# Optimization experiments

Hardware: AMD Instinct MI355X
Metric: run time of the kernel (lower is better)

## Reference

```python
import jax, jax.numpy as jnp
import numpy as np
from jax import lax

D_MODEL = 128
D_INNER = 256   # expand * d_model
D_STATE = 16
D_CONV = 4
DT_RANK = 8     # ceil(d_model / 16)
IN_CH = 64
SCALE = 0.02


def setup_inputs() -> dict:
    key = jax.random.key(0)
    ks = jax.random.split(key, 16)
    r = lambda k, s: jax.random.normal(k, s, dtype=jnp.float32)
    return {
        "x": r(ks[0], (4, IN_CH, 128, 128)),
        "conv_w": r(ks[1], (D_MODEL, IN_CH, 3, 3)) * SCALE,
        "conv_b": r(ks[2], (D_MODEL,)) * SCALE,
        "bn_g": jnp.ones((D_MODEL,), jnp.float32),
        "bn_b": jnp.zeros((D_MODEL,), jnp.float32),
        "bn_mean": r(ks[3], (D_MODEL,)) * SCALE,
        "bn_var": jax.random.uniform(ks[4], (D_MODEL,), jnp.float32) + 0.5,
        "in_w": r(ks[5], (2 * D_INNER, D_MODEL)) * SCALE,
        "conv1d_w": r(ks[6], (D_INNER, 1, D_CONV)) * SCALE,
        "conv1d_b": r(ks[7], (D_INNER,)) * SCALE,
        "xproj_w": r(ks[8], (DT_RANK + 2 * D_STATE, D_INNER)) * SCALE,
        "dtproj_w": r(ks[9], (D_INNER, DT_RANK)) * SCALE,
        "dtproj_b": r(ks[10], (D_INNER,)) * SCALE,
        "A_log": r(ks[11], (D_INNER, D_STATE)) * 0.5,
        "Dp": r(ks[12], (D_INNER,)) * SCALE,
        "out_w": r(ks[13], (D_MODEL, D_INNER)) * SCALE,
    }


def _mamba(u, in_w, conv1d_w, conv1d_b, xproj_w, dtproj_w, dtproj_b, A_log, Dp, out_w):
    # u: [B, L, d_model]
    xz = jnp.einsum("bld,ed->ble", u, in_w)          # [B, L, 2*d_inner]
    x_in, z = jnp.split(xz, 2, axis=-1)
    # depthwise causal conv1d over L
    xc = lax.conv_general_dilated(
        x_in.transpose(0, 2, 1), conv1d_w, (1,), [(D_CONV - 1, 0)],
        dimension_numbers=("NCL", "OIL", "NCL"), feature_group_count=D_INNER,
    ) + conv1d_b[None, :, None]
    x_in = jax.nn.silu(xc).transpose(0, 2, 1)         # [B, L, d_inner]

    x_dbl = jnp.einsum("bld,ed->ble", x_in, xproj_w)  # [B, L, dt_rank+2*d_state]
    dt, Bm, Cm = jnp.split(x_dbl, [DT_RANK, DT_RANK + D_STATE], axis=-1)
    delta = jax.nn.softplus(jnp.einsum("blr,dr->bld", dt, dtproj_w) + dtproj_b)

    A = -jnp.exp(A_log)                               # [d_inner, d_state]
    deltaA = jnp.exp(jnp.einsum("bld,dn->bldn", delta, A))        # [B,L,d,n]
    deltaBu = jnp.einsum("bld,bln,bld->bldn", delta, Bm, x_in)    # [B,L,d,n]

    def step(h, inp):
        dA, dBu, c = inp                              # [B,d,n],[B,d,n],[B,n]
        h = dA * h + dBu
        y = jnp.einsum("bdn,bn->bd", h, c)
        return h, y

    Bsz, L = u.shape[0], u.shape[1]
    h0 = jnp.zeros((Bsz, D_INNER, D_STATE), u.dtype)
    _, ys = lax.scan(step, h0, (deltaA.transpose(1, 0, 2, 3),
                                deltaBu.transpose(1, 0, 2, 3),
                                Cm.transpose(1, 0, 2)))
    y = ys.transpose(1, 0, 2) + x_in * Dp             # [B, L, d_inner]
    y = y * jax.nn.silu(z)
    return jnp.einsum("bld,ed->ble", y, out_w)        # [B, L, d_model]


def reference(x, conv_w, conv_b, bn_g, bn_b, bn_mean, bn_var, in_w, conv1d_w,
              conv1d_b, xproj_w, dtproj_w, dtproj_b, A_log, Dp, out_w):
    # downsample: conv3x3 stride2 + BN(eval) + exact GELU
    y = lax.conv_general_dilated(x, conv_w, (2, 2), [(1, 1), (1, 1)],
                                 dimension_numbers=("NCHW", "OIHW", "NCHW"))
    y = y + conv_b[None, :, None, None]
    inv = bn_g / jnp.sqrt(bn_var + 1e-5)
    y = (y - bn_mean[None, :, None, None]) * inv[None, :, None, None] + bn_b[None, :, None, None]
    y = jax.nn.gelu(y, approximate=False)             # [B, C, H, W]

    B, C, H, W = y.shape
    u = y.reshape(B, C, H * W).transpose(0, 2, 1)     # [B, L, C]
    out = _mamba(u, in_w, conv1d_w, conv1d_b, xproj_w, dtproj_w, dtproj_b,
                 A_log, Dp, out_w)
    out = out.transpose(0, 2, 1).reshape(B, C, H, W)
    return y + out
```

## Files before the change

kernel.cpp:

```cpp
#include <hip/hip_runtime.h>
#include <math.h>

#define NB 4
#define LTOK 4096
#define DM 128
#define DI 256
#define NCH 256
#define TCH 16
#define GSZ 16
#define NG  16

#define OFF_A2     0u
#define OFF_BIAS2  73728u
#define OFF_YDSR   84096u
#define OFF_XPRE   2181248u
#define OFF_Z      6375552u
#define OFF_DELTA  10569856u
#define OFF_YABF   12667008u
#define OFF_BC     14764160u
#define OFF_DSUM   15288448u
#define OFF_GS     15550592u
#define OFF_GD     15812736u
#define OFF_XT     15829120u
#define OFF_WBF    17926272u
#define OFF_WCMP   17963136u
#define OFF_YDSBF  18004096u
#define OFF_INWBF  19052672u
#define OFF_OUTWBF 19085440u

#define DEV __device__ __forceinline__
#define L2E 1.4426950408889634f

typedef short bh8 __attribute__((ext_vector_type(8)));
typedef float f4v __attribute__((ext_vector_type(4)));

DEV float fast_silu(float v) {
  return v * __builtin_amdgcn_rcpf(1.f + __expf(-v));
}

DEV unsigned short f2bf(float f) {
  unsigned int u = __float_as_uint(f);
  u = (u + 0x7FFFu + ((u >> 16) & 1u)) >> 16;
  return (unsigned short)u;
}

DEV float bf2f(unsigned short us) {
  return __uint_as_float((unsigned int)us << 16);
}

__global__ __launch_bounds__(256) void k0_prep(
    const float* __restrict__ conv_w, const float* __restrict__ conv_b,
    const float* __restrict__ bn_g, const float* __restrict__ bn_b,
    const float* __restrict__ bn_mean, const float* __restrict__ bn_var,
    const float* __restrict__ xproj_w, const float* __restrict__ A_log,
    const float* __restrict__ dtw, const float* __restrict__ in_w,
    const float* __restrict__ out_w, float* __restrict__ ws) {
  int i = blockIdx.x * 256 + threadIdx.x;
  if (i < 73728) {
    int ci = i & 63; int tap = (i >> 6) % 9; int co = i / 576;
    float inv = bn_g[co] * rsqrtf(bn_var[co] + 1e-5f);
    ((unsigned short*)(ws + OFF_WBF))[i] = f2bf(conv_w[co * 576 + ci * 9 + tap] * inv);
  } else if (i < 73856) {
    int co = i - 73728;
    float inv = bn_g[co] * rsqrtf(bn_var[co] + 1e-5f);
    ws[OFF_BIAS2 + co] = (conv_b[co] - bn_mean[co]) * inv + bn_b[co];
  } else if (i < 77952) {
    int j = i - 73856;
    ws[OFF_A2 + j] = -__expf(A_log[j]) * L2E;
  } else if (i < 159872) {
    int j = i - 77952;
    int n = j >> 8, k = j & 255;
    float v = 0.f;
    if (n < 256) {
#pragma unroll
      for (int r = 0; r < 8; ++r)
        v = fmaf(dtw[n * 8 + r], xproj_w[r * 256 + k], v);
    } else if (n < 288) {
      v = xproj_w[(8 + n - 256) * 256 + k];
    }
    ((unsigned short*)(ws + OFF_WCMP))[j] = f2bf(v);
  } else if (i < 225408) {
    int j = i - 159872;
    ((unsigned short*)(ws + OFF_INWBF))[j] = f2bf(in_w[j]);
  } else if (i < 258176) {
    int j = i - 225408;
    ((unsigned short*)(ws + OFF_OUTWBF))[j] = f2bf(out_w[j]);
  }
}

__global__ __launch_bounds__(256) void k0b_transpose(
    const float* __restrict__ x, unsigned short* __restrict__ xt) {
  __shared__ float t[64][65];
  const int tid = threadIdx.x;
  const int ixh = blockIdx.x & 1;
  const int iy = (blockIdx.x >> 1) & 127;
  const int b = blockIdx.x >> 8;
  {
    const int ixl = tid & 63, cw = tid >> 6;
#pragma unroll 4
    for (int i = 0; i < 16; ++i) {
      int ci = cw * 16 + i;
      t[ci][ixl] = x[(((size_t)(b * 64 + ci) * 128) + iy) * 128 + ixh * 64 + ixl];
    }
  }
  __syncthreads();
  {
    const int cil = tid & 63, iw = tid >> 6;
    unsigned short* dst = xt + (((size_t)(b * 128 + iy) * 128) + ixh * 64) * 64;
#pragma unroll 4
    for (int i = 0; i < 16; ++i) {
      int ix = iw * 16 + i;
      dst[ix * 64 + cil] = f2bf(t[cil][ix]);
    }
  }
}

__global__ __launch_bounds__(256) void k1_conv_mfma(
    const unsigned short* __restrict__ xt, const unsigned short* __restrict__ wbf,
    const float* __restrict__ bias2, unsigned short* __restrict__ ydsr,
    unsigned short* __restrict__ ydsbf) {
  __shared__ unsigned short ldt[64][66];
  const int tid = threadIdx.x;
  const int lane = tid & 63;
  const int w = tid >> 6;
  const int col = lane & 15, quad = lane >> 4;
  const int cohalf = blockIdx.x & 1;
  const int oy = (blockIdx.x >> 1) & 63;
  const int b = blockIdx.x >> 7;
  const int co0 = cohalf * 64 + (w & 1) * 32;
  const int tok0 = (w >> 1) * 32;
  const int iy0 = 2 * oy - 1;
  const bh8 bzero = {};
  f4v acc[2][2];
#pragma unroll
  for (int mt = 0; mt < 2; ++mt)
#pragma unroll
    for (int nt = 0; nt < 2; ++nt) acc[mt][nt] = (f4v){0.f, 0.f, 0.f, 0.f};

  const unsigned short* ap0 = wbf + (size_t)(co0 + col) * 576;
  const unsigned short* ap1 = wbf + (size_t)(co0 + 16 + col) * 576;

  for (int tap = 0; tap < 9; ++tap) {
    const int kh = tap / 3, kw = tap - kh * 3;
    const int iy = iy0 + kh;
    const int ix0 = 2 * (tok0 + col) - 1 + kw;
    const int ix1 = ix0 + 32;
    const unsigned short* xrow = xt + (long)(b * 128 + iy) * 8192;
    const bool ok0 = (iy >= 0) && (ix0 >= 0);
    const bool ok1 = (iy >= 0);
#pragma unroll
    for (int kc = 0; kc < 2; ++kc) {
      const int cib = kc * 32 + quad * 8;
      bh8 a0 = *(const bh8*)&ap0[tap * 64 + cib];
      bh8 a1 = *(const bh8*)&ap1[tap * 64 + cib];
      bh8 b0 = *(const bh8*)&xrow[(long)ix0 * 64 + cib];
      bh8 b1 = *(const bh8*)&xrow[(long)ix1 * 64 + cib];
      if (!ok0) b0 = bzero;
      if (!ok1) b1 = bzero;
      acc[0][0] = __builtin_amdgcn_mfma_f32_16x16x32_bf16(a0, b0, acc[0][0], 0, 0, 0);
      acc[1][0] = __builtin_amdgcn_mfma_f32_16x16x32_bf16(a1, b0, acc[1][0], 0, 0, 0);
      acc[0][1] = __builtin_amdgcn_mfma_f32_16x16x32_bf16(a0, b1, acc[0][1], 0, 0, 0);
      acc[1][1] = __builtin_amdgcn_mfma_f32_16x16x32_bf16(a1, b1, acc[1][1], 0, 0, 0);
    }
  }
#pragma unroll
  for (int mt = 0; mt < 2; ++mt)
#pragma unroll
    for (int nt = 0; nt < 2; ++nt) {
      const int tok = tok0 + nt * 16 + col;
#pragma unroll
      for (int r = 0; r < 4; ++r) {
        const int co = co0 + mt * 16 + quad * 4 + r;
        float v = acc[mt][nt][r] + bias2[co];
        float g = 0.5f * v * (1.f + erff(v * 0.70710678118f));
        unsigned short gb = f2bf(g);
        ydsr[(((size_t)(b * 128 + co) * 64) + oy) * 64 + tok] = gb;
        ldt[tok][(w & 1) * 32 + mt * 16 + quad * 4 + r] = gb;
      }
    }
  __syncthreads();
  {
    const int tok = tid >> 2, cg = (tid & 3) * 16;
    unsigned short* dst =
        ydsbf + ((size_t)(b * 4096 + oy * 64 + tok)) * 128 + cohalf * 64 + cg;
#pragma unroll
    for (int j = 0; j < 8; ++j)
      ((unsigned int*)dst)[j] = *(const unsigned int*)&ldt[tok][cg + 2 * j];
  }
}

__global__ __launch_bounds__(256) void k2_mfma(
    const unsigned short* __restrict__ ydsbf, const unsigned short* __restrict__ inwbf,
    unsigned short* __restrict__ xpre, unsigned short* __restrict__ z) {
  const int tid = threadIdx.x;
  const int lane = tid & 63;
  const int w = tid >> 6;
  const int col = lane & 15, quad = lane >> 4;
  const int tt = blockIdx.x & 255, b = blockIdx.x >> 8;
  const int t0 = tt * 16;
  bh8 afrag[4];
  {
    const unsigned short* arow = ydsbf + (size_t)(b * 4096 + t0 + col) * 128 + quad * 8;
#pragma unroll
    for (int kb = 0; kb < 4; ++kb) afrag[kb] = *(const bh8*)&arow[kb * 32];
  }
  f4v acc[8];
#pragma unroll
  for (int j = 0; j < 8; ++j) acc[j] = (f4v){0.f, 0.f, 0.f, 0.f};
  const int nt0 = w * 8;
  const unsigned short* wb = inwbf + (size_t)(nt0 * 16 + col) * 128 + quad * 8;
#pragma unroll
  for (int kb = 0; kb < 4; ++kb) {
#pragma unroll
    for (int j = 0; j < 8; ++j) {
      bh8 bfrag = *(const bh8*)&wb[(size_t)j * 2048 + kb * 32];
      acc[j] = __builtin_amdgcn_mfma_f32_16x16x32_bf16(afrag[kb], bfrag, acc[j], 0, 0, 0);
    }
  }
#pragma unroll
  for (int j = 0; j < 8; ++j) {
    const int e = (nt0 + j) * 16 + col;
#pragma unroll
    for (int r = 0; r < 4; ++r) {
      const int t = t0 + quad * 4 + r;
      if (e < 256) xpre[((size_t)(b * 4096 + t)) * 256 + e] = f2bf(acc[j][r]);
      else z[((size_t)(b * 4096 + t)) * 256 + e - 256] = f2bf(acc[j][r]);
    }
  }
}

__global__ __launch_bounds__(256) void k4_mfma(
    const unsigned short* __restrict__ wcomp, const float* __restrict__ dtb,
    const unsigned short* __restrict__ xpre, const float* __restrict__ cw1,
    const float* __restrict__ cb1, unsigned short* __restrict__ xinbf,
    unsigned short* __restrict__ delta, float* __restrict__ bc,
    float* __restrict__ dsum) {
  __shared__ unsigned short ld_xin[16][264];
  __shared__ unsigned short ld_delta[16][264];
  __shared__ float ld_bc[16][33];
  const int tid = threadIdx.x;
  const int lane = tid & 63;
  const int w = tid >> 6;
  const int col = lane & 15, quad = lane >> 4;
  const int tt = blockIdx.x & 255, b = blockIdx.x >> 8;
  const int t0 = tt * 16;

  {
    const int d = tid;
    float4 w4 = *(const float4*)&cw1[d * 4];
    float bias = cb1[d];
    float xw[19];
#pragma unroll
    for (int i = 0; i < 19; ++i) {
      int t = t0 - 3 + i;
      xw[i] = (t >= 0) ? bf2f(xpre[((size_t)(b * 4096 + t)) * 256 + d]) : 0.f;
    }
    unsigned short* dst = xinbf + ((size_t)(b * 4096 + t0)) * 256 + d;
#pragma unroll
    for (int i = 0; i < 16; ++i) {
      float o = bias + w4.x * xw[i] + w4.y * xw[i + 1] + w4.z * xw[i + 2] +
                w4.w * xw[i + 3];
      unsigned short us = f2bf(fast_silu(o));
      ld_xin[i][d] = us;
      dst[(size_t)i * 256] = us;
    }
  }
  __syncthreads();

  bh8 afrag[8];
#pragma unroll
  for (int kb = 0; kb < 8; ++kb)
    afrag[kb] = *(const bh8*)&ld_xin[col][quad * 8 + kb * 32];
  f4v acc[5];
#pragma unroll
  for (int j = 0; j < 5; ++j) acc[j] = (f4v){0.f, 0.f, 0.f, 0.f};

  const int nt0 = w * 5;
  const unsigned short* wb = wcomp + (size_t)(nt0 * 16 + col) * 256 + quad * 8;
#pragma unroll
  for (int kb = 0; kb < 8; ++kb) {
#pragma unroll
    for (int j = 0; j < 5; ++j) {
      bh8 bfrag = *(const bh8*)&wb[(size_t)j * 4096 + kb * 32];
      acc[j] = __builtin_amdgcn_mfma_f32_16x16x32_bf16(afrag[kb], bfrag, acc[j], 0, 0, 0);
    }
  }
#pragma unroll
  for (int j = 0; j < 5; ++j) {
    const int n = (nt0 + j) * 16 + col;
    if (n < 256) {
      float bias = dtb[n];
#pragma unroll
      for (int r = 0; r < 4; ++r) {
        float s = acc[j][r] + bias;
        float dl = fmaxf(s, 0.f) + __logf(1.f + __expf(-fabsf(s)));
        ld_delta[quad * 4 + r][n] = f2bf(dl);
      }
    } else if (n < 288) {
#pragma unroll
      for (int r = 0; r < 4; ++r) ld_bc[quad * 4 + r][n - 256] = acc[j][r];
    }
  }
  __syncthreads();

  {
    float ds = 0.f;
#pragma unroll
    for (int i = 0; i < 16; ++i) ds += bf2f(ld_delta[i][tid]);
    dsum[((size_t)b * 256 + tt) * 256 + tid] = ds;
  }
#pragma unroll
  for (int it = 0; it < 4; ++it) {
    int idx = it * 256 + tid;
    int row = idx >> 6, d4 = (idx & 63) * 4;
    unsigned long long pk = *(const unsigned long long*)&ld_delta[row][d4];
    *(unsigned long long*)&delta[((size_t)(b * 4096 + t0 + row)) * 256 + d4] = pk;
  }
  if (tid < 128) {
    int row = tid >> 3, q = (tid & 7) * 4;
    float4 v = make_float4(ld_bc[row][q], ld_bc[row][q + 1],
                           ld_bc[row][q + 2], ld_bc[row][q + 3]);
    *(float4*)&bc[((size_t)(b * 4096 + t0 + row)) * 32 + q] = v;
  }
}

__global__ __launch_bounds__(256) void k5a_scan1(
    const unsigned short* __restrict__ xinbf, const float* __restrict__ bc,
    const unsigned short* __restrict__ delta, const float* __restrict__ a2tab,
    float* __restrict__ S) {
  __shared__ __align__(16) float bct[TCH * 32];
  const int tid = threadIdx.x;
  const int d = tid;
  const int c = blockIdx.x & (NCH - 1), b = blockIdx.x >> 8;
  const int t0 = c * TCH;
  {
    const float* src = bc + (size_t)(b * 4096 + t0) * 32;
    for (int i = tid; i < TCH * 32; i += 256) bct[i] = src[i];
  }
  float A2[16];
#pragma unroll
  for (int j = 0; j < 4; ++j) {
    float4 a = *(const float4*)&a2tab[d * 16 + j * 4];
    A2[4 * j + 0] = a.x; A2[4 * j + 1] = a.y; A2[4 * j + 2] = a.z; A2[4 * j + 3] = a.w;
  }
  float h[16];
#pragma unroll
  for (int n = 0; n < 16; ++n) h[n] = 0.f;
  const unsigned short* pd = delta + (size_t)(b * 4096 + t0) * 256 + d;
  const unsigned short* px = xinbf + (size_t)(b * 4096 + t0) * 256 + d;
  __syncthreads();
#pragma unroll 4
  for (int i = 0; i < TCH; ++i) {
    float dl = bf2f(pd[(size_t)i * 256]);
    float xv = bf2f(px[(size_t)i * 256]);
    float dlx = dl * xv;
    const float* r = &bct[i * 32];
    float4 B0 = *(const float4*)&r[0];
    float4 B1 = *(const float4*)&r[4];
    float4 B2 = *(const float4*)&r[8];
    float4 B3 = *(const float4*)&r[12];
    float Bv[16] = {B0.x, B0.y, B0.z, B0.w, B1.x, B1.y, B1.z, B1.w,
                    B2.x, B2.y, B2.z, B2.w, B3.x, B3.y, B3.z, B3.w};
#pragma unroll
    for (int n = 0; n < 16; ++n)
      h[n] = fmaf(exp2f(dl * A2[n]), h[n], dlx * Bv[n]);
  }
  const size_t sbase = ((size_t)(b * NCH + c) * 16) * 256 + d;
#pragma unroll
  for (int n = 0; n < 16; ++n) S[sbase + (size_t)n * 256] = h[n];
}

__global__ __launch_bounds__(256) void k5b1_group(
    float* __restrict__ S, const float* __restrict__ dsum,
    const float* __restrict__ a2tab, float* __restrict__ Gs,
    float* __restrict__ Gd) {
  const int d = threadIdx.x;
  const int n = blockIdx.x & 15, g = (blockIdx.x >> 4) & (NG - 1),
            b = blockIdx.x >> 8;
  const float A2 = a2tab[d * 16 + n];
  float h = 0.f, cum = 0.f;
#pragma unroll 4
  for (int c16 = 0; c16 < GSZ; ++c16) {
    int c = g * GSZ + c16;
    size_t si = ((size_t)(b * NCH + c) * 16 + n) * 256 + d;
    float s = S[si];
    float dsv = dsum[((size_t)b * NCH + c) * 256 + d];
    float P = exp2f(A2 * dsv);
    S[si] = h;
    h = fmaf(P, h, s);
    cum += dsv;
  }
  Gs[((size_t)(b * NG + g) * 16 + n) * 256 + d] = h;
  if (n == 0) Gd[((size_t)b * NG + g) * 256 + d] = cum;
}

__global__ __launch_bounds__(256) void k5b2_groupscan(
    float* __restrict__ Gs, const float* __restrict__ Gd,
    const float* __restrict__ a2tab) {
  const int d = threadIdx.x;
  const int n = blockIdx.x & 15, b = blockIdx.x >> 4;
  const float A2 = a2tab[d * 16 + n];
  float h = 0.f;
#pragma unroll
  for (int g = 0; g < NG; ++g) {
    size_t gi = ((size_t)(b * NG + g) * 16 + n) * 256 + d;
    float s = Gs[gi];
    float P = exp2f(A2 * Gd[((size_t)b * NG + g) * 256 + d]);
    Gs[gi] = h;
    h = fmaf(P, h, s);
  }
}

__global__ __launch_bounds__(256) void k5c_scan2(
    const unsigned short* __restrict__ xinbf, const float* __restrict__ bc,
    const unsigned short* __restrict__ delta, const unsigned short* __restrict__ z,
    const float* __restrict__ a2tab, const float* __restrict__ Dp,
    const float* __restrict__ dsum, const float* __restrict__ Gs,
    const float* __restrict__ S, unsigned short* __restrict__ yabf) {
  __shared__ __align__(16) float bct[TCH * 32];
  const int tid = threadIdx.x;
  const int d = tid;
  const int c = blockIdx.x & (NCH - 1), b = blockIdx.x >> 8;
  const int t0 = c * TCH;
  {
    const float* src = bc + (size_t)(b * 4096 + t0) * 32;
    for (int i = tid; i < TCH * 32; i += 256) bct[i] = src[i];
  }
  float A2[16];
#pragma unroll
  for (int j = 0; j < 4; ++j) {
    float4 a = *(const float4*)&a2tab[d * 16 + j * 4];
    A2[4 * j + 0] = a.x; A2[4 * j + 1] = a.y; A2[4 * j + 2] = a.z; A2[4 * j + 3] = a.w;
  }
  const float Dpd = Dp[d];
  const int g = c >> 4, c16 = c & 15;
  float dpref = 0.f;
  {
    const float* pds = dsum + ((size_t)b * NCH + g * GSZ) * 256 + d;
    for (int cc = 0; cc < c16; ++cc) dpref += pds[(size_t)cc * 256];
  }
  const size_t sbase = ((size_t)(b * NCH + c) * 16) * 256 + d;
  const size_t gbase = ((size_t)(b * NG + g) * 16) * 256 + d;
  float h[16];
#pragma unroll
  for (int n = 0; n < 16; ++n) {
    float gi = Gs[gbase + (size_t)n * 256];
    float hl = S[sbase + (size_t)n * 256];
    h[n] = fmaf(exp2f(A2[n] * dpref), gi, hl);
  }
  const size_t base = (size_t)(b * 4096 + t0) * 256 + d;
  const unsigned short* pd = delta + base;
  const unsigned short* px = xinbf + base;
  const unsigned short* pz = z + base;
  unsigned short* py = yabf + base;
  __syncthreads();
#pragma unroll 4
  for (int i = 0; i < TCH; ++i) {
    float dl = bf2f(pd[(size_t)i * 256]);
    float xv = bf2f(px[(size_t)i * 256]);
    float zv = bf2f(pz[(size_t)i * 256]);
    float dlx = dl * xv;
    const float* r = &bct[i * 32];
    float4 B0 = *(const float4*)&r[0];
    float4 B1 = *(const float4*)&r[4];
    float4 B2 = *(const float4*)&r[8];
    float4 B3 = *(const float4*)&r[12];
    float4 C0 = *(const float4*)&r[16];
    float4 C1 = *(const float4*)&r[20];
    float4 C2 = *(const float4*)&r[24];
    float4 C3 = *(const float4*)&r[28];
    float Bv[16] = {B0.x, B0.y, B0.z, B0.w, B1.x, B1.y, B1.z, B1.w,
                    B2.x, B2.y, B2.z, B2.w, B3.x, B3.y, B3.z, B3.w};
    float Cv[16] = {C0.x, C0.y, C0.z, C0.w, C1.x, C1.y, C1.z, C1.w,
                    C2.x, C2.y, C2.z, C2.w, C3.x, C3.y, C3.z, C3.w};
    float y = 0.f;
#pragma unroll
    for (int n = 0; n < 16; ++n) {
      h[n] = fmaf(exp2f(dl * A2[n]), h[n], dlx * Bv[n]);
      y = fmaf(h[n], Cv[n], y);
    }
    py[(size_t)i * 256] = f2bf((y + xv * Dpd) * fast_silu(zv));
  }
}

__global__ __launch_bounds__(256) void k6_mfma(
    const unsigned short* __restrict__ yabf, const unsigned short* __restrict__ outwbf,
    const unsigned short* __restrict__ ydsr, float* __restrict__ out) {
  __shared__ float ld[16][132];
  const int tid = threadIdx.x;
  const int lane = tid & 63;
  const int w = tid >> 6;
  const int col = lane & 15, quad = lane >> 4;
  const int tt = blockIdx.x & 255, b = blockIdx.x >> 8;
  const int t0 = tt * 16;
  const int oy = t0 >> 6, ox0 = t0 & 63;
  bh8 afrag[8];
  {
    const unsigned short* arow = yabf + (size_t)(b * 4096 + t0 + col) * 256 + quad * 8;
#pragma unroll
    for (int kb = 0; kb < 8; ++kb) afrag[kb] = *(const bh8*)&arow[kb * 32];
  }
  f4v acc[2];
#pragma unroll
  for (int j = 0; j < 2; ++j) acc[j] = (f4v){0.f, 0.f, 0.f, 0.f};
  const int nt0 = w * 2;
  const unsigned short* wb = outwbf + (size_t)(nt0 * 16 + col) * 256 + quad * 8;
#pragma unroll
  for (int kb = 0; kb < 8; ++kb) {
#pragma unroll
    for (int j = 0; j < 2; ++j) {
      bh8 bfrag = *(const bh8*)&wb[(size_t)j * 4096 + kb * 32];
      acc[j] = __builtin_amdgcn_mfma_f32_16x16x32_bf16(afrag[kb], bfrag, acc[j], 0, 0, 0);
    }
  }
#pragma unroll
  for (int j = 0; j < 2; ++j)
#pragma unroll
    for (int r = 0; r < 4; ++r)
      ld[quad * 4 + r][(nt0 + j) * 16 + col] = acc[j][r];
  __syncthreads();
  {
    const int cc = tid >> 1, half = tid & 1;
    size_t base = (((size_t)(b * 128 + cc) * 64) + oy) * 64 + ox0 + half * 8;
    const unsigned short* rp = ydsr + base;
    const int m0 = half * 8;
    float4 o0 = make_float4(ld[m0 + 0][cc] + bf2f(rp[0]), ld[m0 + 1][cc] + bf2f(rp[1]),
                            ld[m0 + 2][cc] + bf2f(rp[2]), ld[m0 + 3][cc] + bf2f(rp[3]));
    float4 o1 = make_float4(ld[m0 + 4][cc] + bf2f(rp[4]), ld[m0 + 5][cc] + bf2f(rp[5]),
                            ld[m0 + 6][cc] + bf2f(rp[6]), ld[m0 + 7][cc] + bf2f(rp[7]));
    *(float4*)&out[base] = o0;
    *(float4*)&out[base + 4] = o1;
  }
}

extern "C" void kernel_launch(void* const* d_in, const int* in_sizes, int n_in,
                              void* d_out, int out_size, void* d_ws, size_t ws_size,
                              hipStream_t stream) {
  (void)in_sizes; (void)n_in; (void)out_size; (void)ws_size;
  const float* x        = (const float*)d_in[0];
  const float* conv_w   = (const float*)d_in[1];
  const float* conv_b   = (const float*)d_in[2];
  const float* bn_g     = (const float*)d_in[3];
  const float* bn_b     = (const float*)d_in[4];
  const float* bn_mean  = (const float*)d_in[5];
  const float* bn_var   = (const float*)d_in[6];
  const float* in_w     = (const float*)d_in[7];
  const float* conv1d_w = (const float*)d_in[8];
  const float* conv1d_b = (const float*)d_in[9];
  const float* xproj_w  = (const float*)d_in[10];
  const float* dtproj_w = (const float*)d_in[11];
  const float* dtproj_b = (const float*)d_in[12];
  const float* A_log    = (const float*)d_in[13];
  const float* Dp       = (const float*)d_in[14];
  const float* out_w    = (const float*)d_in[15];
  float* ws = (float*)d_ws;
  float* out = (float*)d_out;

  k0_prep<<<1009, 256, 0, stream>>>(conv_w, conv_b, bn_g, bn_b, bn_mean, bn_var,
                                    xproj_w, A_log, dtproj_w, in_w, out_w, ws);
  k0b_transpose<<<1024, 256, 0, stream>>>(x, (unsigned short*)(ws + OFF_XT));
  k1_conv_mfma<<<512, 256, 0, stream>>>((const unsigned short*)(ws + OFF_XT),
                                        (const unsigned short*)(ws + OFF_WBF),
                                        ws + OFF_BIAS2,
                                        (unsigned short*)(ws + OFF_YDSR),
                                        (unsigned short*)(ws + OFF_YDSBF));
  k2_mfma<<<1024, 256, 0, stream>>>((const unsigned short*)(ws + OFF_YDSBF),
                                    (const unsigned short*)(ws + OFF_INWBF),
                                    (unsigned short*)(ws + OFF_XPRE),
                                    (unsigned short*)(ws + OFF_Z));
  k4_mfma<<<1024, 256, 0, stream>>>((const unsigned short*)(ws + OFF_WCMP),
                                    dtproj_b,
                                    (const unsigned short*)(ws + OFF_XPRE),
                                    conv1d_w, conv1d_b,
                                    (unsigned short*)(ws + OFF_XT),
                                    (unsigned short*)(ws + OFF_DELTA),
                                    ws + OFF_BC, ws + OFF_DSUM);
  k5a_scan1<<<1024, 256, 0, stream>>>((const unsigned short*)(ws + OFF_XT),
                                      ws + OFF_BC,
                                      (const unsigned short*)(ws + OFF_DELTA),
                                      ws + OFF_A2, ws + OFF_XPRE);
  k5b1_group<<<1024, 256, 0, stream>>>(ws + OFF_XPRE, ws + OFF_DSUM, ws + OFF_A2,
                                       ws + OFF_GS, ws + OFF_GD);
  k5b2_groupscan<<<64, 256, 0, stream>>>(ws + OFF_GS, ws + OFF_GD, ws + OFF_A2);
  k5c_scan2<<<1024, 256, 0, stream>>>((const unsigned short*)(ws + OFF_XT),
                                      ws + OFF_BC,
                                      (const unsigned short*)(ws + OFF_DELTA),
                                      (const unsigned short*)(ws + OFF_Z),
                                      ws + OFF_A2, Dp, ws + OFF_DSUM,
                                      ws + OFF_GS, ws + OFF_XPRE,
                                      (unsigned short*)(ws + OFF_YABF));
  k6_mfma<<<1024, 256, 0, stream>>>((const unsigned short*)(ws + OFF_YABF),
                                    (const unsigned short*)(ws + OFF_OUTWBF),
                                    (const unsigned short*)(ws + OFF_YDSR), out);
}
```

Measured before the change: 241.3 us.

## Fuse chunk scan into projection kernel and output GEMM into final scan

Moves the first-pass per-chunk selective scan into the x-projection kernel so delta, x and B are read from shared memory instead of being re-read from global memory. It also fuses the second-pass scan with the output projection GEMM, keeping y in LDS instead of writing and re-reading a bf16 buffer. Chunk delta prefix sums are precomputed in the group kernel, and the group scans preload their inputs into registers. This removes two launches and several global round trips, at the cost of more registers and shared memory per block and a reshuffled workspace layout that reuses the freed buffers.

Result: faster. 215.7 us (-10.6%).

```diff
diff --git a/kernel.cpp b/kernel.cpp
--- a/kernel.cpp
+++ b/kernel.cpp
@@ -14,9 +14,10 @@
 #define OFF_BIAS2  73728u
 #define OFF_YDSR   84096u
 #define OFF_XPRE   2181248u
+#define OFF_S0     4278400u
 #define OFF_Z      6375552u
 #define OFF_DELTA  10569856u
-#define OFF_YABF   12667008u
+#define OFF_S1     12667008u
 #define OFF_BC     14764160u
 #define OFF_DSUM   15288448u
 #define OFF_GS     15550592u
@@ -25,6 +26,7 @@
 #define OFF_WBF    17926272u
 #define OFF_WCMP   17963136u
 #define OFF_YDSBF  18004096u
+#define OFF_DPREF  18004096u
 #define OFF_INWBF  19052672u
 #define OFF_OUTWBF 19085440u
 
@@ -229,12 +231,13 @@
   }
 }
 
-__global__ __launch_bounds__(256) void k4_mfma(
+__global__ __launch_bounds__(256) void k45_mfma(
     const unsigned short* __restrict__ wcomp, const float* __restrict__ dtb,
     const unsigned short* __restrict__ xpre, const float* __restrict__ cw1,
-    const float* __restrict__ cb1, unsigned short* __restrict__ xinbf,
-    unsigned short* __restrict__ delta, float* __restrict__ bc,
-    float* __restrict__ dsum) {
+    const float* __restrict__ cb1, const float* __restrict__ a2tab,
+    unsigned short* __restrict__ xinbf, unsigned short* __restrict__ delta,
+    float* __restrict__ bc, float* __restrict__ dsum,
+    float* __restrict__ S0, float* __restrict__ S1) {
   __shared__ unsigned short ld_xin[16][264];
   __shared__ unsigned short ld_delta[16][264];
   __shared__ float ld_bc[16][33];
@@ -267,48 +270,75 @@
   }
   __syncthreads();
 
-  bh8 afrag[8];
-#pragma unroll
-  for (int kb = 0; kb < 8; ++kb)
-    afrag[kb] = *(const bh8*)&ld_xin[col][quad * 8 + kb * 32];
-  f4v acc[5];
-#pragma unroll
-  for (int j = 0; j < 5; ++j) acc[j] = (f4v){0.f, 0.f, 0.f, 0.f};
-
-  const int nt0 = w * 5;
-  const unsigned short* wb = wcomp + (size_t)(nt0 * 16 + col) * 256 + quad * 8;
-#pragma unroll
-  for (int kb = 0; kb < 8; ++kb) {
+  {
+    bh8 afrag[8];
+#pragma unroll
+    for (int kb = 0; kb < 8; ++kb)
+      afrag[kb] = *(const bh8*)&ld_xin[col][quad * 8 + kb * 32];
+    f4v acc[5];
+#pragma unroll
+    for (int j = 0; j < 5; ++j) acc[j] = (f4v){0.f, 0.f, 0.f, 0.f};
+
+    const int nt0 = w * 5;
+    const unsigned short* wb = wcomp + (size_t)(nt0 * 16 + col) * 256 + quad * 8;
+#pragma unroll
+    for (int kb = 0; kb < 8; ++kb) {
+#pragma unroll
+      for (int j = 0; j < 5; ++j) {
+        bh8 bfrag = *(const bh8*)&wb[(size_t)j * 4096 + kb * 32];
+        acc[j] = __builtin_amdgcn_mfma_f32_16x16x32_bf16(afrag[kb], bfrag, acc[j], 0, 0, 0);
+      }
+    }
 #pragma unroll
     for (int j = 0; j < 5; ++j) {
-      bh8 bfrag = *(const bh8*)&wb[(size_t)j * 4096 + kb * 32];
-      acc[j] = __builtin_amdgcn_mfma_f32_16x16x32_bf16(afrag[kb], bfrag, acc[j], 0, 0, 0);
-    }
-  }
-#pragma unroll
-  for (int j = 0; j < 5; ++j) {
-    const int n = (nt0 + j) * 16 + col;
-    if (n < 256) {
-      float bias = dtb[n];
-#pragma unroll
-      for (int r = 0; r < 4; ++r) {
-        float s = acc[j][r] + bias;
-        float dl = fmaxf(s, 0.f) + __logf(1.f + __expf(-fabsf(s)));
-        ld_delta[quad * 4 + r][n] = f2bf(dl);
+      const int n = (nt0 + j) * 16 + col;
+      if (n < 256) {
+        float bias = dtb[n];
+#pragma unroll
+        for (int r = 0; r < 4; ++r) {
+          float s = acc[j][r] + bias;
+          float dl = fmaxf(s, 0.f) + __logf(1.f + __expf(-fabsf(s)));
+          ld_delta[quad * 4 + r][n] = f2bf(dl);
+        }
+      } else if (n < 288) {
+#pragma unroll
+        for (int r = 0; r < 4; ++r) ld_bc[quad * 4 + r][n - 256] = acc[j][r];
       }
-    } else if (n < 288) {
-#pragma unroll
-      for (int r = 0; r < 4; ++r) ld_bc[quad * 4 + r][n - 256] = acc[j][r];
-    }
-  }
-  __syncthreads();
-
-  {
+    }
+  }
+  __syncthreads();
+
+  {
+    const int d = tid;
+    float A2[16];
+#pragma unroll
+    for (int j = 0; j < 4; ++j) {
+      float4 a = *(const float4*)&a2tab[d * 16 + j * 4];
+      A2[4 * j + 0] = a.x; A2[4 * j + 1] = a.y;
+      A2[4 * j + 2] = a.z; A2[4 * j + 3] = a.w;
+    }
+    float h[16];
+#pragma unroll
+    for (int n = 0; n < 16; ++n) h[n] = 0.f;
     float ds = 0.f;
-#pragma unroll
-    for (int i = 0; i < 16; ++i) ds += bf2f(ld_delta[i][tid]);
-    dsum[((size_t)b * 256 + tt) * 256 + tid] = ds;
-  }
+#pragma unroll 4
+    for (int i = 0; i < TCH; ++i) {
+      float dl = bf2f(ld_delta[i][d]);
+      float xv = bf2f(ld_xin[i][d]);
+      ds += dl;
+      float dlx = dl * xv;
+#pragma unroll
+      for (int n = 0; n < 16; ++n)
+        h[n] = fmaf(exp2f(dl * A2[n]), h[n], dlx * ld_bc[i][n]);
+    }
+    dsum[((size_t)b * NCH + tt) * 256 + d] = ds;
+    float* S = (b & 2) ? (S1 + (size_t)(b & 1) * 1048576)
+                       : (S0 + (size_t)(b & 1) * 1048576);
+    const size_t sbase = ((size_t)tt * 16) * 256 + d;
+#pragma unroll
+    for (int n = 0; n < 16; ++n) S[sbase + (size_t)n * 256] = h[n];
+  }
+
 #pragma unroll
   for (int it = 0; it < 4; ++it) {
     int idx = it * 256 + tid;
@@ -324,71 +354,32 @@
   }
 }
 
-__global__ __launch_bounds__(256) void k5a_scan1(
-    const unsigned short* __restrict__ xinbf, const float* __restrict__ bc,
-    const unsigned short* __restrict__ delta, const float* __restrict__ a2tab,
-    float* __restrict__ S) {
-  __shared__ __align__(16) float bct[TCH * 32];
-  const int tid = threadIdx.x;
-  const int d = tid;
-  const int c = blockIdx.x & (NCH - 1), b = blockIdx.x >> 8;
-  const int t0 = c * TCH;
-  {
-    const float* src = bc + (size_t)(b * 4096 + t0) * 32;
-    for (int i = tid; i < TCH * 32; i += 256) bct[i] = src[i];
-  }
-  float A2[16];
-#pragma unroll
-  for (int j = 0; j < 4; ++j) {
-    float4 a = *(const float4*)&a2tab[d * 16 + j * 4];
-    A2[4 * j + 0] = a.x; A2[4 * j + 1] = a.y; A2[4 * j + 2] = a.z; A2[4 * j + 3] = a.w;
-  }
-  float h[16];
-#pragma unroll
-  for (int n = 0; n < 16; ++n) h[n] = 0.f;
-  const unsigned short* pd = delta + (size_t)(b * 4096 + t0) * 256 + d;
-  const unsigned short* px = xinbf + (size_t)(b * 4096 + t0) * 256 + d;
-  __syncthreads();
-#pragma unroll 4
-  for (int i = 0; i < TCH; ++i) {
-    float dl = bf2f(pd[(size_t)i * 256]);
-    float xv = bf2f(px[(size_t)i * 256]);
-    float dlx = dl * xv;
-    const float* r = &bct[i * 32];
-    float4 B0 = *(const float4*)&r[0];
-    float4 B1 = *(const float4*)&r[4];
-    float4 B2 = *(const float4*)&r[8];
-    float4 B3 = *(const float4*)&r[12];
-    float Bv[16] = {B0.x, B0.y, B0.z, B0.w, B1.x, B1.y, B1.z, B1.w,
-                    B2.x, B2.y, B2.z, B2.w, B3.x, B3.y, B3.z, B3.w};
-#pragma unroll
-    for (int n = 0; n < 16; ++n)
-      h[n] = fmaf(exp2f(dl * A2[n]), h[n], dlx * Bv[n]);
-  }
-  const size_t sbase = ((size_t)(b * NCH + c) * 16) * 256 + d;
-#pragma unroll
-  for (int n = 0; n < 16; ++n) S[sbase + (size_t)n * 256] = h[n];
-}
-
 __global__ __launch_bounds__(256) void k5b1_group(
-    float* __restrict__ S, const float* __restrict__ dsum,
-    const float* __restrict__ a2tab, float* __restrict__ Gs,
-    float* __restrict__ Gd) {
+    float* __restrict__ S0, float* __restrict__ S1,
+    const float* __restrict__ dsum, const float* __restrict__ a2tab,
+    float* __restrict__ Gs, float* __restrict__ Gd,
+    float* __restrict__ dpref) {
   const int d = threadIdx.x;
   const int n = blockIdx.x & 15, g = (blockIdx.x >> 4) & (NG - 1),
             b = blockIdx.x >> 8;
+  float* S = (b & 2) ? (S1 + (size_t)(b & 1) * 1048576)
+                     : (S0 + (size_t)(b & 1) * 1048576);
   const float A2 = a2tab[d * 16 + n];
+  const size_t s0 = ((size_t)(g * GSZ) * 16 + n) * 256 + d;
+  const size_t d0 = ((size_t)b * NCH + g * GSZ) * 256 + d;
+  float sv[GSZ], dv[GSZ];
+#pragma unroll
+  for (int k = 0; k < GSZ; ++k) {
+    sv[k] = S[s0 + (size_t)k * 4096];
+    dv[k] = dsum[d0 + (size_t)k * 256];
+  }
   float h = 0.f, cum = 0.f;
-#pragma unroll 4
-  for (int c16 = 0; c16 < GSZ; ++c16) {
-    int c = g * GSZ + c16;
-    size_t si = ((size_t)(b * NCH + c) * 16 + n) * 256 + d;
-    float s = S[si];
-    float dsv = dsum[((size_t)b * NCH + c) * 256 + d];
-    float P = exp2f(A2 * dsv);
-    S[si] = h;
-    h = fmaf(P, h, s);
-    cum += dsv;
+#pragma unroll
+  for (int k = 0; k < GSZ; ++k) {
+    S[s0 + (size_t)k * 4096] = h;
+    if (n == 0) dpref[d0 + (size_t)k * 256] = cum;
+    h = fmaf(exp2f(A2 * dv[k]), h, sv[k]);
+    cum += dv[k];
   }
   Gs[((size_t)(b * NG + g) * 16 + n) * 256 + d] = h;
   if (n == 0) Gd[((size_t)b * NG + g) * 256 + d] = cum;
@@ -400,24 +391,33 @@
   const int d = threadIdx.x;
   const int n = blockIdx.x & 15, b = blockIdx.x >> 4;
   const float A2 = a2tab[d * 16 + n];
+  float sv[NG], dv[NG];
+  const size_t g0 = ((size_t)(b * NG) * 16 + n) * 256 + d;
+  const size_t gd0 = (size_t)b * NG * 256 + d;
+#pragma unroll
+  for (int g = 0; g < NG; ++g) {
+    sv[g] = Gs[g0 + (size_t)g * 4096];
+    dv[g] = Gd[gd0 + (size_t)g * 256];
+  }
   float h = 0.f;
 #pragma unroll
   for (int g = 0; g < NG; ++g) {
-    size_t gi = ((size_t)(b * NG + g) * 16 + n) * 256 + d;
-    float s = Gs[gi];
-    float P = exp2f(A2 * Gd[((size_t)b * NG + g) * 256 + d]);
-    Gs[gi] = h;
-    h = fmaf(P, h, s);
-  }
-}
-
-__global__ __launch_bounds__(256) void k5c_scan2(
+    Gs[g0 + (size_t)g * 4096] = h;
+    h = fmaf(exp2f(A2 * dv[g]), h, sv[g]);
+  }
+}
+
+__global__ __launch_bounds__(256) void k56_fused(
     const unsigned short* __restrict__ xinbf, const float* __restrict__ bc,
     const unsigned short* __restrict__ delta, const unsigned short* __restrict__ z,
     const float* __restrict__ a2tab, const float* __restrict__ Dp,
-    const float* __restrict__ dsum, const float* __restrict__ Gs,
-    const float* __restrict__ S, unsigned short* __restrict__ yabf) {
+    const float* __restrict__ dpref, const float* __restrict__ Gs,
+    const float* __restrict__ S0, const float* __restrict__ S1,
+    const unsigned short* __restrict__ outwbf, const unsigned short* __restrict__ ydsr,
+    float* __restrict__ out) {
   __shared__ __align__(16) float bct[TCH * 32];
+  __shared__ __align__(16) unsigned short ld_y[16][264];
+  __shared__ float ldo[16][132];
   const int tid = threadIdx.x;
   const int d = tid;
   const int c = blockIdx.x & (NCH - 1), b = blockIdx.x >> 8;
@@ -430,29 +430,27 @@
 #pragma unroll
   for (int j = 0; j < 4; ++j) {
     float4 a = *(const float4*)&a2tab[d * 16 + j * 4];
-    A2[4 * j + 0] = a.x; A2[4 * j + 1] = a.y; A2[4 * j + 2] = a.z; A2[4 * j + 3] = a.w;
+    A2[4 * j + 0] = a.x; A2[4 * j + 1] = a.y;
+    A2[4 * j + 2] = a.z; A2[4 * j + 3] = a.w;
   }
   const float Dpd = Dp[d];
-  const int g = c >> 4, c16 = c & 15;
-  float dpref = 0.f;
-  {
-    const float* pds = dsum + ((size_t)b * NCH + g * GSZ) * 256 + d;
-    for (int cc = 0; cc < c16; ++cc) dpref += pds[(size_t)cc * 256];
-  }
-  const size_t sbase = ((size_t)(b * NCH + c) * 16) * 256 + d;
+  const int g = c >> 4;
+  const float dp0 = dpref[((size_t)b * NCH + c) * 256 + d];
+  const float* S = (b & 2) ? (S1 + (size_t)(b & 1) * 1048576)
+                           : (S0 + (size_t)(b & 1) * 1048576);
+  const size_t sbase = ((size_t)c * 16) * 256 + d;
   const size_t gbase = ((size_t)(b * NG + g) * 16) * 256 + d;
   float h[16];
 #pragma unroll
   for (int n = 0; n < 16; ++n) {
     float gi = Gs[gbase + (size_t)n * 256];
     float hl = S[sbase + (size_t)n * 256];
-    h[n] = fmaf(exp2f(A2[n] * dpref), gi, hl);
+    h[n] = fmaf(exp2f(A2[n] * dp0), gi, hl);
   }
   const size_t base = (size_t)(b * 4096 + t0) * 256 + d;
   const unsigned short* pd = delta + base;
   const unsigned short* px = xinbf + base;
   const unsigned short* pz = z + base;
-  unsigned short* py = yabf + base;
   __syncthreads();
 #pragma unroll 4
   for (int i = 0; i < TCH; ++i) {
@@ -479,27 +477,18 @@
       h[n] = fmaf(exp2f(dl * A2[n]), h[n], dlx * Bv[n]);
       y = fmaf(h[n], Cv[n], y);
     }
-    py[(size_t)i * 256] = f2bf((y + xv * Dpd) * fast_silu(zv));
-  }
-}
-
-__global__ __launch_bounds__(256) void k6_mfma(
-    const unsigned short* __restrict__ yabf, const unsigned short* __restrict__ outwbf,
-    const unsigned short* __restrict__ ydsr, float* __restrict__ out) {
-  __shared__ float ld[16][132];
-  const int tid = threadIdx.x;
+    ld_y[i][d] = f2bf((y + xv * Dpd) * fast_silu(zv));
+  }
+  __syncthreads();
+
   const int lane = tid & 63;
   const int w = tid >> 6;
   const int col = lane & 15, quad = lane >> 4;
-  const int tt = blockIdx.x & 255, b = blockIdx.x >> 8;
-  const int t0 = tt * 16;
   const int oy = t0 >> 6, ox0 = t0 & 63;
   bh8 afrag[8];
-  {
-    const unsigned short* arow = yabf + (size_t)(b * 4096 + t0 + col) * 256 + quad * 8;
-#pragma unroll
-    for (int kb = 0; kb < 8; ++kb) afrag[kb] = *(const bh8*)&arow[kb * 32];
-  }
+#pragma unroll
+  for (int kb = 0; kb < 8; ++kb)
+    afrag[kb] = *(const bh8*)&ld_y[col][quad * 8 + kb * 32];
   f4v acc[2];
 #pragma unroll
   for (int j = 0; j < 2; ++j) acc[j] = (f4v){0.f, 0.f, 0.f, 0.f};
@@ -517,19 +506,19 @@
   for (int j = 0; j < 2; ++j)
 #pragma unroll
     for (int r = 0; r < 4; ++r)
-      ld[quad * 4 + r][(nt0 + j) * 16 + col] = acc[j][r];
+      ldo[quad * 4 + r][(nt0 + j) * 16 + col] = acc[j][r];
   __syncthreads();
   {
     const int cc = tid >> 1, half = tid & 1;
-    size_t base = (((size_t)(b * 128 + cc) * 64) + oy) * 64 + ox0 + half * 8;
-    const unsigned short* rp = ydsr + base;
+    size_t obase = (((size_t)(b * 128 + cc) * 64) + oy) * 64 + ox0 + half * 8;
+    const unsigned short* rp = ydsr + obase;
     const int m0 = half * 8;
-    float4 o0 = make_float4(ld[m0 + 0][cc] + bf2f(rp[0]), ld[m0 + 1][cc] + bf2f(rp[1]),
-                            ld[m0 + 2][cc] + bf2f(rp[2]), ld[m0 + 3][cc] + bf2f(rp[3]));
-    float4 o1 = make_float4(ld[m0 + 4][cc] + bf2f(rp[4]), ld[m0 + 5][cc] + bf2f(rp[5]),
-                            ld[m0 + 6][cc] + bf2f(rp[6]), ld[m0 + 7][cc] + bf2f(rp[7]));
-    *(float4*)&out[base] = o0;
-    *(float4*)&out[base + 4] = o1;
+    float4 o0 = make_float4(ldo[m0 + 0][cc] + bf2f(rp[0]), ldo[m0 + 1][cc] + bf2f(rp[1]),
+                            ldo[m0 + 2][cc] + bf2f(rp[2]), ldo[m0 + 3][cc] + bf2f(rp[3]));
+    float4 o1 = make_float4(ldo[m0 + 4][cc] + bf2f(rp[4]), ldo[m0 + 5][cc] + bf2f(rp[5]),
+                            ldo[m0 + 6][cc] + bf2f(rp[6]), ldo[m0 + 7][cc] + bf2f(rp[7]));
+    *(float4*)&out[obase] = o0;
+    *(float4*)&out[obase + 4] = o1;
   }
 }
 
@@ -568,28 +557,24 @@
                                     (const unsigned short*)(ws + OFF_INWBF),
                                     (unsigned short*)(ws + OFF_XPRE),
                                     (unsigned short*)(ws + OFF_Z));
-  k4_mfma<<<1024, 256, 0, stream>>>((const unsigned short*)(ws + OFF_WCMP),
-                                    dtproj_b,
-                                    (const unsigned short*)(ws + OFF_XPRE),
-                                    conv1d_w, conv1d_b,
-                                    (unsigned short*)(ws + OFF_XT),
-                                    (unsigned short*)(ws + OFF_DELTA),
-                                    ws + OFF_BC, ws + OFF_DSUM);
-  k5a_scan1<<<1024, 256, 0, stream>>>((const unsigned short*)(ws + OFF_XT),
-                                      ws + OFF_BC,
-                                      (const unsigned short*)(ws + OFF_DELTA),
-                                      ws + OFF_A2, ws + OFF_XPRE);
-  k5b1_group<<<1024, 256, 0, stream>>>(ws + OFF_XPRE, ws + OFF_DSUM, ws + OFF_A2,
-                                       ws + OFF_GS, ws + OFF_GD);
+  k45_mfma<<<1024, 256, 0, stream>>>((const unsigned short*)(ws + OFF_WCMP),
+                                     dtproj_b,
+                                     (const unsigned short*)(ws + OFF_XPRE),
+                                     conv1d_w, conv1d_b, ws + OFF_A2,
+                                     (unsigned short*)(ws + OFF_XT),
+                                     (unsigned short*)(ws + OFF_DELTA),
+                                     ws + OFF_BC, ws + OFF_DSUM,
+                                     ws + OFF_S0, ws + OFF_S1);
+  k5b1_group<<<1024, 256, 0, stream>>>(ws + OFF_S0, ws + OFF_S1, ws + OFF_DSUM,
+                                       ws + OFF_A2, ws + OFF_GS, ws + OFF_GD,
+                                       ws + OFF_DPREF);
   k5b2_groupscan<<<64, 256, 0, stream>>>(ws + OFF_GS, ws + OFF_GD, ws + OFF_A2);
-  k5c_scan2<<<1024, 256, 0, stream>>>((const unsigned short*)(ws + OFF_XT),
+  k56_fused<<<1024, 256, 0, stream>>>((const unsigned short*)(ws + OFF_XT),
                                       ws + OFF_BC,
                                       (const unsigned short*)(ws + OFF_DELTA),
                                       (const unsigned short*)(ws + OFF_Z),
-                                      ws + OFF_A2, Dp, ws + OFF_DSUM,
-                                      ws + OFF_GS, ws + OFF_XPRE,
-                                      (unsigned short*)(ws + OFF_YABF));
-  k6_mfma<<<1024, 256, 0, stream>>>((const unsigned short*)(ws + OFF_YABF),
-                                    (const unsigned short*)(ws + OFF_OUTWBF),
-                                    (const unsigned short*)(ws + OFF_YDSR), out);
-}
+                                      ws + OFF_A2, Dp, ws + OFF_DPREF,
+                                      ws + OFF_GS, ws + OFF_S0, ws + OFF_S1,
+                                      (const unsigned short*)(ws + OFF_OUTWBF),
+                                      (const unsigned short*)(ws + OFF_YDSR), out);
+}
```
